# Kernel optimization log

Hardware: AMD Instinct MI355X
Metric: run time of the kernel (lower is better)

Reference implementation:

```python
import jax, jax.numpy as jnp
import numpy as np
import math

B, SQ, SK, D_MODEL, OUT_DIM = 8, 2048, 2048, 1024, 128
MASK_VALUE = -1e6  # torch code fills masked scores with -1000000.0, not -inf


def setup_inputs() -> dict:
    key = jax.random.key(0)
    ks = jax.random.split(key, 10)
    scale = 1.0 / math.sqrt(D_MODEL)
    return {
        "queries": jax.random.normal(ks[0], (B, SQ, D_MODEL), dtype=jnp.float32),
        "keys": jax.random.normal(ks[1], (B, SK, D_MODEL), dtype=jnp.float32),
        "values": jax.random.normal(ks[2], (B, SK, D_MODEL), dtype=jnp.float32),
        "valid_lens": jax.random.randint(ks[3], (B,), 1, SK + 1, dtype=jnp.int32),
        "w_q": jax.random.normal(ks[4], (D_MODEL, OUT_DIM), dtype=jnp.float32) * scale,
        "b_q": jnp.zeros((OUT_DIM,), dtype=jnp.float32),
        "w_k": jax.random.normal(ks[5], (D_MODEL, OUT_DIM), dtype=jnp.float32) * scale,
        "b_k": jnp.zeros((OUT_DIM,), dtype=jnp.float32),
        "w_v": jax.random.normal(ks[6], (D_MODEL, OUT_DIM), dtype=jnp.float32) * scale,
        "b_v": jnp.zeros((OUT_DIM,), dtype=jnp.float32),
    }


def reference(queries, keys, values, valid_lens, w_q, b_q, w_k, b_k, w_v, b_v):
    # QKV projections (LazyLinear equivalents)
    Q = queries @ w_q + b_q   # [B, SQ, OUT_DIM]
    K = keys @ w_k + b_k      # [B, SK, OUT_DIM]
    V = values @ w_v + b_v    # [B, SK, OUT_DIM]
    dim = Q.shape[-1]
    scores = jnp.einsum("bqd,bkd->bqk", Q, K) / jnp.sqrt(jnp.asarray(dim, Q.dtype))
    # masked_softmax: valid_lens [B] -> mask positions >= valid_len on the key axis
    mask = jnp.arange(scores.shape[-1])[None, None, :] < valid_lens[:, None, None]
    scores = jnp.where(mask, scores, jnp.asarray(MASK_VALUE, scores.dtype))
    attn = jax.nn.softmax(scores, axis=-1)
    return jnp.einsum("bqk,bkd->bqd", attn, V)  # [B, SQ, OUT_DIM]
```

## Files before the change

### kernel.cpp

```cpp
#include <hip/hip_runtime.h>
#include <math.h>

constexpr int BATCH  = 8;
constexpr int SEQQ   = 2048;
constexpr int SEQK   = 2048;
constexpr int DMODEL = 1024;
constexpr int ODIM   = 128;
constexpr int KSPLIT = 2;

typedef __attribute__((ext_vector_type(8))) short bf16x8;
typedef __attribute__((ext_vector_type(4))) float f32x4;

__device__ inline unsigned short f2bf(float f) {
    union { float f; unsigned int u; } v; v.f = f;
    unsigned int r = v.u + 0x7FFFu + ((v.u >> 16) & 1u);
    return (unsigned short)(r >> 16);
}

__device__ __forceinline__ void gl_lds16(const void* g, void* l) {
    __builtin_amdgcn_global_load_lds(
        (const __attribute__((address_space(1))) unsigned int*)g,
        (__attribute__((address_space(3))) unsigned int*)l, 16, 0, 0);
}

__global__ __launch_bounds__(256)
void wtrans_kernel(const float* __restrict__ Wq, const float* __restrict__ Wk,
                   const float* __restrict__ Wv, unsigned short* __restrict__ Wt)
{
    const int which = blockIdx.z;
    const float* __restrict__ W = which == 0 ? Wq : (which == 1 ? Wk : Wv);
    unsigned short* __restrict__ dst = Wt + (size_t)which * DMODEL * ODIM;
    const int k0 = blockIdx.x * 32, n0 = blockIdx.y * 32;
    __shared__ unsigned short T[32][36];
    const int t = threadIdx.x;
    const int r = t >> 3, c = (t & 7) * 4;
    float4 w = *(const float4*)(W + (size_t)(k0 + r) * ODIM + n0 + c);
    T[r][c + 0] = f2bf(w.x); T[r][c + 1] = f2bf(w.y);
    T[r][c + 2] = f2bf(w.z); T[r][c + 3] = f2bf(w.w);
    __syncthreads();
    const int n = t >> 3, k4 = (t & 7) * 4;
    ushort4 o;
    o.x = T[k4 + 0][n]; o.y = T[k4 + 1][n];
    o.z = T[k4 + 2][n]; o.w = T[k4 + 3][n];
    *(ushort4*)(dst + (size_t)(n0 + n) * DMODEL + k0 + k4) = o;
}

__global__ __launch_bounds__(256)
void proj_kernel(const float* __restrict__ Aq, const float* __restrict__ Ak,
                 const float* __restrict__ Av,
                 const unsigned short* __restrict__ Wt_all,
                 const float* __restrict__ bq, const float* __restrict__ bk,
                 const float* __restrict__ bv,
                 unsigned short* __restrict__ Qb, unsigned short* __restrict__ Kb,
                 unsigned short* __restrict__ Vt)
{
    const int which = blockIdx.y;
    const float* __restrict__ A    = which == 0 ? Aq : (which == 1 ? Ak : Av);
    const float* __restrict__ bias = which == 0 ? bq : (which == 1 ? bk : bv);
    const unsigned short* __restrict__ Wt = Wt_all + (size_t)which * DMODEL * ODIM;

    const int row0 = blockIdx.x * 64;
    const int t = threadIdx.x, wave = t >> 6, lane = t & 63;
    const int lrow = lane & 15, quad = lane >> 4;

    __shared__ __align__(16) float          As[64][64];
    __shared__ __align__(16) unsigned short Ws[128][64];

    f32x4 acc[8];
#pragma unroll
    for (int nt = 0; nt < 8; ++nt)
#pragma unroll
        for (int i = 0; i < 4; ++i) acc[nt][i] = 0.f;

    const float* agp[4]; float* aldst[4];
    const unsigned short* wgp[4]; unsigned short* wldst[4];
#pragma unroll
    for (int j = 0; j < 4; ++j) {
        const int s = wave * 256 + j * 64 + lane;
        const int ar = s >> 4, ac = s & 15, ag = ac ^ (ar & 7);
        agp[j]   = A + (size_t)(row0 + ar) * DMODEL + ag * 4;
        aldst[j] = &((float*)As)[s * 4];
        const int wr = s >> 3, wc = s & 7, wg = wc ^ (wr & 7);
        wgp[j]   = Wt + (size_t)wr * DMODEL + wg * 8;
        wldst[j] = &((unsigned short*)Ws)[s * 8];
    }

    const int R = wave * 16 + lrow;
    const int x3 = lrow & 7;

    for (int k0 = 0; k0 < DMODEL; k0 += 64) {
#pragma unroll
        for (int j = 0; j < 4; ++j) {
            gl_lds16(agp[j] + k0, aldst[j]);
            gl_lds16(wgp[j] + k0, wldst[j]);
        }
        __syncthreads();
#pragma unroll
        for (int ks = 0; ks < 2; ++ks) {
            const int c0 = ks * 8 + quad * 2;
            float4 a0 = *(const float4*)&As[R][(c0 ^ x3) * 4];
            float4 a1 = *(const float4*)&As[R][((c0 + 1) ^ x3) * 4];
            bf16x8 af;
            af[0] = (short)f2bf(a0.x); af[1] = (short)f2bf(a0.y);
            af[2] = (short)f2bf(a0.z); af[3] = (short)f2bf(a0.w);
            af[4] = (short)f2bf(a1.x); af[5] = (short)f2bf(a1.y);
            af[6] = (short)f2bf(a1.z); af[7] = (short)f2bf(a1.w);
#pragma unroll
            for (int nt = 0; nt < 8; ++nt) {
                const int n = nt * 16 + lrow;
                const int c = (ks * 4 + quad) ^ x3;
                bf16x8 bfr = *(const bf16x8*)&Ws[n][c * 8];
                acc[nt] = __builtin_amdgcn_mfma_f32_16x16x32_bf16(af, bfr, acc[nt], 0, 0, 0);
            }
        }
        __syncthreads();
    }

    const float sc = (which == 0) ? 0.08838834764831845f : 1.0f;
    float bv_[8];
#pragma unroll
    for (int nt = 0; nt < 8; ++nt) bv_[nt] = bias[nt * 16 + lrow];

    const int b  = row0 >> 11;
    const int mb = row0 & 2047;

    if (which == 2) {
#pragma unroll
        for (int nt = 0; nt < 8; ++nt) {
            const int n = nt * 16 + lrow;
            ushort4 o;
            o.x = f2bf(acc[nt][0] + bv_[nt]);
            o.y = f2bf(acc[nt][1] + bv_[nt]);
            o.z = f2bf(acc[nt][2] + bv_[nt]);
            o.w = f2bf(acc[nt][3] + bv_[nt]);
            *(ushort4*)(Vt + ((size_t)b * ODIM + n) * SEQK + mb + wave * 16 + quad * 4) = o;
        }
    } else {
        unsigned short* __restrict__ Ob = (which == 0) ? Qb : Kb;
#pragma unroll
        for (int nt = 0; nt < 8; ++nt)
#pragma unroll
            for (int r = 0; r < 4; ++r) {
                float val = sc * (acc[nt][r] + bv_[nt]);
                Ob[(size_t)(row0 + wave * 16 + quad * 4 + r) * ODIM + nt * 16 + lrow] = f2bf(val);
            }
    }
}

__global__ __launch_bounds__(256)
void flash_kernel(const unsigned short* __restrict__ Qb,
                  const unsigned short* __restrict__ Kb,
                  const unsigned short* __restrict__ Vt,
                  const int* __restrict__ valid_lens,
                  float* __restrict__ Op, float* __restrict__ Lp)
{
    const int b = blockIdx.y, s = blockIdx.z, q0 = blockIdx.x * 64;
    const int t = threadIdx.x, wave = t >> 6, lane = t & 63;
    const int lrow = lane & 15, quad = lane >> 4;
    const int SKH = SEQK / KSPLIT;

    const int valid = valid_lens[b];
    const int vloc  = min(valid - s * SKH, SKH);

    float* __restrict__ opart = Op + ((size_t)(s * BATCH + b) * SEQQ + q0) * ODIM;
    float* __restrict__ lpart = Lp + (size_t)(s * BATCH + b) * SEQQ + q0;

    if (vloc <= 0) {
        float4 z = {0.f, 0.f, 0.f, 0.f};
#pragma unroll
        for (int i = 0; i < 8; ++i) ((float4*)opart)[i * 256 + t] = z;
        if (t < 64) lpart[t] = 0.f;
        return;
    }

    __shared__ __align__(16) unsigned short Ks[64][136];
    __shared__ __align__(16) unsigned short Vs[128][72];
    __shared__ __align__(16) unsigned short Ps[4][16][72];

    bf16x8 qf[4];
    {
        const unsigned short* qptr =
            Qb + ((size_t)b * SEQQ + q0 + wave * 16 + lrow) * ODIM + quad * 8;
#pragma unroll
        for (int ks = 0; ks < 4; ++ks) qf[ks] = *(const bf16x8*)(qptr + ks * 32);
    }

    f32x4 o[8];
#pragma unroll
    for (int nt = 0; nt < 8; ++nt)
#pragma unroll
        for (int i = 0; i < 4; ++i) o[nt][i] = 0.f;
    float lsum[4] = {0.f, 0.f, 0.f, 0.f};

    const unsigned short* kbase = Kb + ((size_t)b * SEQK + s * SKH) * ODIM;
    const unsigned short* vbase = Vt + (size_t)b * ODIM * SEQK + s * SKH;

    const int kr = t >> 2, kc = (t & 3) * 32;
    const int vr = t >> 1, vc = (t & 1) * 32;
    const int nch = (vloc + 63) >> 6;

    for (int c = 0; c < nch; ++c) {
        const int k0 = c * 64;
        {
            const unsigned short* ksrc = kbase + (size_t)(k0 + kr) * ODIM + kc;
            const unsigned short* vsrc = vbase + (size_t)vr * SEQK + k0 + vc;
#pragma unroll
            for (int i = 0; i < 4; ++i) {
                *(int4*)&Ks[kr][kc + i * 8] = *(const int4*)(ksrc + i * 8);
                *(int4*)&Vs[vr][vc + i * 8] = *(const int4*)(vsrc + i * 8);
            }
        }
        __syncthreads();

        f32x4 sv[4];
#pragma unroll
        for (int nt = 0; nt < 4; ++nt)
#pragma unroll
            for (int i = 0; i < 4; ++i) sv[nt][i] = 0.f;
#pragma unroll
        for (int ks = 0; ks < 4; ++ks)
#pragma unroll
            for (int nt = 0; nt < 4; ++nt) {
                bf16x8 kf = *(const bf16x8*)&Ks[nt * 16 + lrow][ks * 32 + quad * 8];
                sv[nt] = __builtin_amdgcn_mfma_f32_16x16x32_bf16(qf[ks], kf, sv[nt], 0, 0, 0);
            }

        if (k0 + 64 > vloc) {
#pragma unroll
            for (int nt = 0; nt < 4; ++nt)
                if (k0 + nt * 16 + lrow >= vloc) {
#pragma unroll
                    for (int i = 0; i < 4; ++i) sv[nt][i] = -1e30f;
                }
        }

#pragma unroll
        for (int nt = 0; nt < 4; ++nt)
#pragma unroll
            for (int r = 0; r < 4; ++r) {
                float p = __expf(sv[nt][r]);
                lsum[r] += p;
                Ps[wave][quad * 4 + r][nt * 16 + lrow] = f2bf(p);
            }

        bf16x8 pf0 = *(const bf16x8*)&Ps[wave][lrow][quad * 8];
        bf16x8 pf1 = *(const bf16x8*)&Ps[wave][lrow][32 + quad * 8];

#pragma unroll
        for (int nt = 0; nt < 8; ++nt) {
            bf16x8 vf0 = *(const bf16x8*)&Vs[nt * 16 + lrow][quad * 8];
            o[nt] = __builtin_amdgcn_mfma_f32_16x16x32_bf16(pf0, vf0, o[nt], 0, 0, 0);
        }
#pragma unroll
        for (int nt = 0; nt < 8; ++nt) {
            bf16x8 vf1 = *(const bf16x8*)&Vs[nt * 16 + lrow][32 + quad * 8];
            o[nt] = __builtin_amdgcn_mfma_f32_16x16x32_bf16(pf1, vf1, o[nt], 0, 0, 0);
        }
        __syncthreads();
    }

#pragma unroll
    for (int msk = 1; msk < 16; msk <<= 1)
#pragma unroll
        for (int r = 0; r < 4; ++r) lsum[r] += __shfl_xor(lsum[r], msk);
    if (lrow == 0) {
#pragma unroll
        for (int r = 0; r < 4; ++r)
            lpart[wave * 16 + quad * 4 + r] = lsum[r];
    }

#pragma unroll
    for (int nt = 0; nt < 8; ++nt)
#pragma unroll
        for (int r = 0; r < 4; ++r)
            opart[(size_t)(wave * 16 + quad * 4 + r) * ODIM + nt * 16 + lrow] = o[nt][r];
}

__global__ __launch_bounds__(256)
void combine_kernel(const float* __restrict__ Op, const float* __restrict__ Lp,
                    float* __restrict__ out)
{
    const int idx = blockIdx.x * 256 + threadIdx.x;
    const int row = idx >> 5;
    const size_t stride = (size_t)BATCH * SEQQ;
    float l = Lp[row] + Lp[stride + row];
    const float inv = 1.f / l;
    float4 a = ((const float4*)Op)[idx];
    float4 c = ((const float4*)(Op + stride * ODIM))[idx];
    float4 r;
    r.x = (a.x + c.x) * inv; r.y = (a.y + c.y) * inv;
    r.z = (a.z + c.z) * inv; r.w = (a.w + c.w) * inv;
    ((float4*)out)[idx] = r;
}

extern "C" void kernel_launch(void* const* d_in, const int* in_sizes, int n_in,
                              void* d_out, int out_size, void* d_ws, size_t ws_size,
                              hipStream_t stream)
{
    const float* queries    = (const float*)d_in[0];
    const float* keys       = (const float*)d_in[1];
    const float* values     = (const float*)d_in[2];
    const int*   valid_lens = (const int*)d_in[3];
    const float* w_q        = (const float*)d_in[4];
    const float* b_q        = (const float*)d_in[5];
    const float* w_k        = (const float*)d_in[6];
    const float* b_k        = (const float*)d_in[7];
    const float* w_v        = (const float*)d_in[8];
    const float* b_v        = (const float*)d_in[9];
    float* out = (float*)d_out;

    const size_t nQKV = (size_t)BATCH * SEQQ * ODIM;
    unsigned short* Qb = (unsigned short*)d_ws;
    unsigned short* Kb = Qb + nQKV;
    unsigned short* Vt = Kb + nQKV;
    unsigned short* Wt = Vt + nQKV;
    float* Op = (float*)(Wt + (size_t)3 * DMODEL * ODIM);
    float* Lp = Op + (size_t)KSPLIT * nQKV;

    wtrans_kernel<<<dim3(DMODEL / 32, ODIM / 32, 3), 256, 0, stream>>>(w_q, w_k, w_v, Wt);

    proj_kernel<<<dim3((BATCH * SEQQ) / 64, 3), 256, 0, stream>>>(
        queries, keys, values, Wt, b_q, b_k, b_v, Qb, Kb, Vt);

    flash_kernel<<<dim3(SEQQ / 64, BATCH, KSPLIT), 256, 0, stream>>>(
        Qb, Kb, Vt, valid_lens, Op, Lp);

    combine_kernel<<<(BATCH * SEQQ * ODIM / 4) / 256, 256, 0, stream>>>(Op, Lp, out);
}
```

Measured before the change: 266.9 us.

## Drop LDS staging in projection and flash kernels, widen tiles, split keys four ways

The projection kernel stops staging A and W through LDS and reads fragments straight from global memory. Each wave now computes a 32x64 tile and uses a packed round-to-bf16 conversion. The flash kernel handles 128 query rows per block (32 per wave), reads K and V fragments directly from global memory with no block barriers, and splits the key axis four ways when workspace allows. Fully masked splits skip writing the O partials, and the combine kernel ignores splits whose row sum is zero. The aim is to cut LDS traffic and barriers and to increase parallelism, at the cost of more L2/global traffic from uncoalesced fragment loads and a larger combine pass.

```diff
diff --git a/kernel.cpp b/kernel.cpp
--- a/kernel.cpp
+++ b/kernel.cpp
@@ -6,7 +6,6 @@
 constexpr int SEQK   = 2048;
 constexpr int DMODEL = 1024;
 constexpr int ODIM   = 128;
-constexpr int KSPLIT = 2;
 
 typedef __attribute__((ext_vector_type(8))) short bf16x8;
 typedef __attribute__((ext_vector_type(4))) float f32x4;
@@ -17,10 +16,10 @@
     return (unsigned short)(r >> 16);
 }
 
-__device__ __forceinline__ void gl_lds16(const void* g, void* l) {
-    __builtin_amdgcn_global_load_lds(
-        (const __attribute__((address_space(1))) unsigned int*)g,
-        (__attribute__((address_space(3))) unsigned int*)l, 16, 0, 0);
+__device__ __forceinline__ unsigned int pk2bf(float a, float b) {
+    unsigned int ua = __float_as_uint(a) + 0x8000u;
+    unsigned int ub = __float_as_uint(b) + 0x8000u;
+    return __builtin_amdgcn_perm(ub, ua, 0x07060302u);
 }
 
 __global__ __launch_bounds__(256)
@@ -62,167 +61,152 @@
     const int row0 = blockIdx.x * 64;
     const int t = threadIdx.x, wave = t >> 6, lane = t & 63;
     const int lrow = lane & 15, quad = lane >> 4;
-
-    __shared__ __align__(16) float          As[64][64];
-    __shared__ __align__(16) unsigned short Ws[128][64];
-
-    f32x4 acc[8];
-#pragma unroll
-    for (int nt = 0; nt < 8; ++nt)
-#pragma unroll
-        for (int i = 0; i < 4; ++i) acc[nt][i] = 0.f;
-
-    const float* agp[4]; float* aldst[4];
-    const unsigned short* wgp[4]; unsigned short* wldst[4];
-#pragma unroll
-    for (int j = 0; j < 4; ++j) {
-        const int s = wave * 256 + j * 64 + lane;
-        const int ar = s >> 4, ac = s & 15, ag = ac ^ (ar & 7);
-        agp[j]   = A + (size_t)(row0 + ar) * DMODEL + ag * 4;
-        aldst[j] = &((float*)As)[s * 4];
-        const int wr = s >> 3, wc = s & 7, wg = wc ^ (wr & 7);
-        wgp[j]   = Wt + (size_t)wr * DMODEL + wg * 8;
-        wldst[j] = &((unsigned short*)Ws)[s * 8];
-    }
-
-    const int R = wave * 16 + lrow;
-    const int x3 = lrow & 7;
-
-    for (int k0 = 0; k0 < DMODEL; k0 += 64) {
-#pragma unroll
-        for (int j = 0; j < 4; ++j) {
-            gl_lds16(agp[j] + k0, aldst[j]);
-            gl_lds16(wgp[j] + k0, wldst[j]);
+    const int mh = (wave & 1) * 32;
+    const int nh = (wave >> 1) * 64;
+
+    const float* a0 = A + (size_t)(row0 + mh + lrow) * DMODEL + quad * 8;
+    const float* a1 = a0 + (size_t)16 * DMODEL;
+    const unsigned short* w0 = Wt + (size_t)(nh + lrow) * DMODEL + quad * 8;
+
+    f32x4 acc[2][4];
+#pragma unroll
+    for (int mt = 0; mt < 2; ++mt)
+#pragma unroll
+        for (int nt = 0; nt < 4; ++nt)
+#pragma unroll
+            for (int i = 0; i < 4; ++i) acc[mt][nt][i] = 0.f;
+
+#pragma unroll 4
+    for (int k0 = 0; k0 < DMODEL; k0 += 32) {
+        float4 x0 = *(const float4*)(a0 + k0);
+        float4 x1 = *(const float4*)(a0 + k0 + 4);
+        float4 y0 = *(const float4*)(a1 + k0);
+        float4 y1 = *(const float4*)(a1 + k0 + 4);
+        bf16x8 af0, af1;
+        ((unsigned int*)&af0)[0] = pk2bf(x0.x, x0.y);
+        ((unsigned int*)&af0)[1] = pk2bf(x0.z, x0.w);
+        ((unsigned int*)&af0)[2] = pk2bf(x1.x, x1.y);
+        ((unsigned int*)&af0)[3] = pk2bf(x1.z, x1.w);
+        ((unsigned int*)&af1)[0] = pk2bf(y0.x, y0.y);
+        ((unsigned int*)&af1)[1] = pk2bf(y0.z, y0.w);
+        ((unsigned int*)&af1)[2] = pk2bf(y1.x, y1.y);
+        ((unsigned int*)&af1)[3] = pk2bf(y1.z, y1.w);
+#pragma unroll
+        for (int nt = 0; nt < 4; ++nt) {
+            bf16x8 wf = *(const bf16x8*)(w0 + (size_t)nt * 16 * DMODEL + k0);
+            acc[0][nt] = __builtin_amdgcn_mfma_f32_16x16x32_bf16(af0, wf, acc[0][nt], 0, 0, 0);
+            acc[1][nt] = __builtin_amdgcn_mfma_f32_16x16x32_bf16(af1, wf, acc[1][nt], 0, 0, 0);
         }
-        __syncthreads();
-#pragma unroll
-        for (int ks = 0; ks < 2; ++ks) {
-            const int c0 = ks * 8 + quad * 2;
-            float4 a0 = *(const float4*)&As[R][(c0 ^ x3) * 4];
-            float4 a1 = *(const float4*)&As[R][((c0 + 1) ^ x3) * 4];
-            bf16x8 af;
-            af[0] = (short)f2bf(a0.x); af[1] = (short)f2bf(a0.y);
-            af[2] = (short)f2bf(a0.z); af[3] = (short)f2bf(a0.w);
-            af[4] = (short)f2bf(a1.x); af[5] = (short)f2bf(a1.y);
-            af[6] = (short)f2bf(a1.z); af[7] = (short)f2bf(a1.w);
-#pragma unroll
-            for (int nt = 0; nt < 8; ++nt) {
-                const int n = nt * 16 + lrow;
-                const int c = (ks * 4 + quad) ^ x3;
-                bf16x8 bfr = *(const bf16x8*)&Ws[n][c * 8];
-                acc[nt] = __builtin_amdgcn_mfma_f32_16x16x32_bf16(af, bfr, acc[nt], 0, 0, 0);
-            }
-        }
-        __syncthreads();
     }
 
     const float sc = (which == 0) ? 0.08838834764831845f : 1.0f;
-    float bv_[8];
-#pragma unroll
-    for (int nt = 0; nt < 8; ++nt) bv_[nt] = bias[nt * 16 + lrow];
+    float bv_[4];
+#pragma unroll
+    for (int nt = 0; nt < 4; ++nt) bv_[nt] = bias[nh + nt * 16 + lrow];
 
     const int b  = row0 >> 11;
     const int mb = row0 & 2047;
 
     if (which == 2) {
 #pragma unroll
-        for (int nt = 0; nt < 8; ++nt) {
-            const int n = nt * 16 + lrow;
-            ushort4 o;
-            o.x = f2bf(acc[nt][0] + bv_[nt]);
-            o.y = f2bf(acc[nt][1] + bv_[nt]);
-            o.z = f2bf(acc[nt][2] + bv_[nt]);
-            o.w = f2bf(acc[nt][3] + bv_[nt]);
-            *(ushort4*)(Vt + ((size_t)b * ODIM + n) * SEQK + mb + wave * 16 + quad * 4) = o;
-        }
+        for (int mt = 0; mt < 2; ++mt)
+#pragma unroll
+            for (int nt = 0; nt < 4; ++nt) {
+                const int n = nh + nt * 16 + lrow;
+                ushort4 o;
+                o.x = f2bf(acc[mt][nt][0] + bv_[nt]);
+                o.y = f2bf(acc[mt][nt][1] + bv_[nt]);
+                o.z = f2bf(acc[mt][nt][2] + bv_[nt]);
+                o.w = f2bf(acc[mt][nt][3] + bv_[nt]);
+                *(ushort4*)(Vt + ((size_t)b * ODIM + n) * SEQK
+                            + mb + mh + mt * 16 + quad * 4) = o;
+            }
     } else {
         unsigned short* __restrict__ Ob = (which == 0) ? Qb : Kb;
 #pragma unroll
-        for (int nt = 0; nt < 8; ++nt)
-#pragma unroll
-            for (int r = 0; r < 4; ++r) {
-                float val = sc * (acc[nt][r] + bv_[nt]);
-                Ob[(size_t)(row0 + wave * 16 + quad * 4 + r) * ODIM + nt * 16 + lrow] = f2bf(val);
-            }
-    }
-}
-
-__global__ __launch_bounds__(256)
+        for (int mt = 0; mt < 2; ++mt)
+#pragma unroll
+            for (int nt = 0; nt < 4; ++nt)
+#pragma unroll
+                for (int r = 0; r < 4; ++r) {
+                    float val = sc * (acc[mt][nt][r] + bv_[nt]);
+                    Ob[(size_t)(row0 + mh + mt * 16 + quad * 4 + r) * ODIM
+                       + nh + nt * 16 + lrow] = f2bf(val);
+                }
+    }
+}
+
+__global__ __launch_bounds__(256, 2)
 void flash_kernel(const unsigned short* __restrict__ Qb,
                   const unsigned short* __restrict__ Kb,
                   const unsigned short* __restrict__ Vt,
                   const int* __restrict__ valid_lens,
-                  float* __restrict__ Op, float* __restrict__ Lp)
-{
-    const int b = blockIdx.y, s = blockIdx.z, q0 = blockIdx.x * 64;
+                  float* __restrict__ Op, float* __restrict__ Lp, int nsplit)
+{
+    const int b = blockIdx.y, s = blockIdx.z, q0 = blockIdx.x * 128;
+    const int skh = SEQK / nsplit;
     const int t = threadIdx.x, wave = t >> 6, lane = t & 63;
     const int lrow = lane & 15, quad = lane >> 4;
-    const int SKH = SEQK / KSPLIT;
 
     const int valid = valid_lens[b];
-    const int vloc  = min(valid - s * SKH, SKH);
-
+    const int vloc  = min(valid - s * skh, skh);
+
+    float* __restrict__ lpart = Lp + (size_t)(s * BATCH + b) * SEQQ + q0;
     float* __restrict__ opart = Op + ((size_t)(s * BATCH + b) * SEQQ + q0) * ODIM;
-    float* __restrict__ lpart = Lp + (size_t)(s * BATCH + b) * SEQQ + q0;
 
     if (vloc <= 0) {
-        float4 z = {0.f, 0.f, 0.f, 0.f};
-#pragma unroll
-        for (int i = 0; i < 8; ++i) ((float4*)opart)[i * 256 + t] = z;
-        if (t < 64) lpart[t] = 0.f;
+        if (lane < 32) lpart[wave * 32 + lane] = 0.f;
         return;
     }
 
-    __shared__ __align__(16) unsigned short Ks[64][136];
-    __shared__ __align__(16) unsigned short Vs[128][72];
-    __shared__ __align__(16) unsigned short Ps[4][16][72];
-
-    bf16x8 qf[4];
+    __shared__ __align__(16) unsigned short Ps[4][32][72];
+
+    const int r0 = q0 + wave * 32;
+
+    bf16x8 qf[2][4];
     {
-        const unsigned short* qptr =
-            Qb + ((size_t)b * SEQQ + q0 + wave * 16 + lrow) * ODIM + quad * 8;
-#pragma unroll
-        for (int ks = 0; ks < 4; ++ks) qf[ks] = *(const bf16x8*)(qptr + ks * 32);
-    }
-
-    f32x4 o[8];
-#pragma unroll
-    for (int nt = 0; nt < 8; ++nt)
-#pragma unroll
-        for (int i = 0; i < 4; ++i) o[nt][i] = 0.f;
-    float lsum[4] = {0.f, 0.f, 0.f, 0.f};
-
-    const unsigned short* kbase = Kb + ((size_t)b * SEQK + s * SKH) * ODIM;
-    const unsigned short* vbase = Vt + (size_t)b * ODIM * SEQK + s * SKH;
-
-    const int kr = t >> 2, kc = (t & 3) * 32;
-    const int vr = t >> 1, vc = (t & 1) * 32;
+        const unsigned short* qp =
+            Qb + ((size_t)b * SEQQ + r0 + lrow) * ODIM + quad * 8;
+#pragma unroll
+        for (int mt = 0; mt < 2; ++mt)
+#pragma unroll
+            for (int ks = 0; ks < 4; ++ks)
+                qf[mt][ks] = *(const bf16x8*)(qp + (size_t)mt * 16 * ODIM + ks * 32);
+    }
+
+    f32x4 o[2][8];
+#pragma unroll
+    for (int mt = 0; mt < 2; ++mt)
+#pragma unroll
+        for (int nt = 0; nt < 8; ++nt)
+#pragma unroll
+            for (int i = 0; i < 4; ++i) o[mt][nt][i] = 0.f;
+    float lsum[2][4] = {{0.f, 0.f, 0.f, 0.f}, {0.f, 0.f, 0.f, 0.f}};
+
+    const unsigned short* kb =
+        Kb + ((size_t)b * SEQK + s * skh + lrow) * ODIM + quad * 8;
+    const unsigned short* vb =
+        Vt + (size_t)b * ODIM * SEQK + (size_t)lrow * SEQK + s * skh + quad * 8;
+
     const int nch = (vloc + 63) >> 6;
 
     for (int c = 0; c < nch; ++c) {
         const int k0 = c * 64;
-        {
-            const unsigned short* ksrc = kbase + (size_t)(k0 + kr) * ODIM + kc;
-            const unsigned short* vsrc = vbase + (size_t)vr * SEQK + k0 + vc;
-#pragma unroll
-            for (int i = 0; i < 4; ++i) {
-                *(int4*)&Ks[kr][kc + i * 8] = *(const int4*)(ksrc + i * 8);
-                *(int4*)&Vs[vr][vc + i * 8] = *(const int4*)(vsrc + i * 8);
-            }
-        }
-        __syncthreads();
-
-        f32x4 sv[4];
-#pragma unroll
-        for (int nt = 0; nt < 4; ++nt)
-#pragma unroll
-            for (int i = 0; i < 4; ++i) sv[nt][i] = 0.f;
+
+        f32x4 sv[2][4];
+#pragma unroll
+        for (int mt = 0; mt < 2; ++mt)
+#pragma unroll
+            for (int nt = 0; nt < 4; ++nt)
+#pragma unroll
+                for (int i = 0; i < 4; ++i) sv[mt][nt][i] = 0.f;
 #pragma unroll
         for (int ks = 0; ks < 4; ++ks)
 #pragma unroll
             for (int nt = 0; nt < 4; ++nt) {
-                bf16x8 kf = *(const bf16x8*)&Ks[nt * 16 + lrow][ks * 32 + quad * 8];
-                sv[nt] = __builtin_amdgcn_mfma_f32_16x16x32_bf16(qf[ks], kf, sv[nt], 0, 0, 0);
+                bf16x8 kf = *(const bf16x8*)(kb + (size_t)(k0 + nt * 16) * ODIM + ks * 32);
+                sv[0][nt] = __builtin_amdgcn_mfma_f32_16x16x32_bf16(qf[0][ks], kf, sv[0][nt], 0, 0, 0);
+                sv[1][nt] = __builtin_amdgcn_mfma_f32_16x16x32_bf16(qf[1][ks], kf, sv[1][nt], 0, 0, 0);
             }
 
         if (k0 + 64 > vloc) {
@@ -230,66 +214,83 @@
             for (int nt = 0; nt < 4; ++nt)
                 if (k0 + nt * 16 + lrow >= vloc) {
 #pragma unroll
-                    for (int i = 0; i < 4; ++i) sv[nt][i] = -1e30f;
+                    for (int i = 0; i < 4; ++i) { sv[0][nt][i] = -1e30f; sv[1][nt][i] = -1e30f; }
                 }
         }
 
 #pragma unroll
-        for (int nt = 0; nt < 4; ++nt)
-#pragma unroll
-            for (int r = 0; r < 4; ++r) {
-                float p = __expf(sv[nt][r]);
-                lsum[r] += p;
-                Ps[wave][quad * 4 + r][nt * 16 + lrow] = f2bf(p);
+        for (int mt = 0; mt < 2; ++mt)
+#pragma unroll
+            for (int nt = 0; nt < 4; ++nt)
+#pragma unroll
+                for (int r = 0; r < 4; ++r) {
+                    float p = __expf(sv[mt][nt][r]);
+                    lsum[mt][r] += p;
+                    Ps[wave][mt * 16 + quad * 4 + r][nt * 16 + lrow] =
+                        (unsigned short)((__float_as_uint(p) + 0x8000u) >> 16);
+                }
+
+        bf16x8 pf[2][2];
+#pragma unroll
+        for (int mt = 0; mt < 2; ++mt) {
+            pf[mt][0] = *(const bf16x8*)&Ps[wave][mt * 16 + lrow][quad * 8];
+            pf[mt][1] = *(const bf16x8*)&Ps[wave][mt * 16 + lrow][32 + quad * 8];
+        }
+
+#pragma unroll
+        for (int k2 = 0; k2 < 2; ++k2)
+#pragma unroll
+            for (int nt = 0; nt < 8; ++nt) {
+                bf16x8 vf = *(const bf16x8*)(vb + (size_t)(nt * 16) * SEQK + k0 + k2 * 32);
+                o[0][nt] = __builtin_amdgcn_mfma_f32_16x16x32_bf16(pf[0][k2], vf, o[0][nt], 0, 0, 0);
+                o[1][nt] = __builtin_amdgcn_mfma_f32_16x16x32_bf16(pf[1][k2], vf, o[1][nt], 0, 0, 0);
             }
-
-        bf16x8 pf0 = *(const bf16x8*)&Ps[wave][lrow][quad * 8];
-        bf16x8 pf1 = *(const bf16x8*)&Ps[wave][lrow][32 + quad * 8];
-
-#pragma unroll
-        for (int nt = 0; nt < 8; ++nt) {
-            bf16x8 vf0 = *(const bf16x8*)&Vs[nt * 16 + lrow][quad * 8];
-            o[nt] = __builtin_amdgcn_mfma_f32_16x16x32_bf16(pf0, vf0, o[nt], 0, 0, 0);
-        }
-#pragma unroll
-        for (int nt = 0; nt < 8; ++nt) {
-            bf16x8 vf1 = *(const bf16x8*)&Vs[nt * 16 + lrow][32 + quad * 8];
-            o[nt] = __builtin_amdgcn_mfma_f32_16x16x32_bf16(pf1, vf1, o[nt], 0, 0, 0);
-        }
-        __syncthreads();
     }
 
 #pragma unroll
     for (int msk = 1; msk < 16; msk <<= 1)
 #pragma unroll
-        for (int r = 0; r < 4; ++r) lsum[r] += __shfl_xor(lsum[r], msk);
+        for (int mt = 0; mt < 2; ++mt)
+#pragma unroll
+            for (int r = 0; r < 4; ++r) lsum[mt][r] += __shfl_xor(lsum[mt][r], msk);
     if (lrow == 0) {
 #pragma unroll
-        for (int r = 0; r < 4; ++r)
-            lpart[wave * 16 + quad * 4 + r] = lsum[r];
-    }
-
-#pragma unroll
-    for (int nt = 0; nt < 8; ++nt)
-#pragma unroll
-        for (int r = 0; r < 4; ++r)
-            opart[(size_t)(wave * 16 + quad * 4 + r) * ODIM + nt * 16 + lrow] = o[nt][r];
+        for (int mt = 0; mt < 2; ++mt)
+#pragma unroll
+            for (int r = 0; r < 4; ++r)
+                lpart[wave * 32 + mt * 16 + quad * 4 + r] = lsum[mt][r];
+    }
+
+#pragma unroll
+    for (int mt = 0; mt < 2; ++mt)
+#pragma unroll
+        for (int nt = 0; nt < 8; ++nt)
+#pragma unroll
+            for (int r = 0; r < 4; ++r)
+                opart[(size_t)(wave * 32 + mt * 16 + quad * 4 + r) * ODIM
+                      + nt * 16 + lrow] = o[mt][nt][r];
 }
 
 __global__ __launch_bounds__(256)
 void combine_kernel(const float* __restrict__ Op, const float* __restrict__ Lp,
-                    float* __restrict__ out)
+                    float* __restrict__ out, int nsplit)
 {
     const int idx = blockIdx.x * 256 + threadIdx.x;
     const int row = idx >> 5;
-    const size_t stride = (size_t)BATCH * SEQQ;
-    float l = Lp[row] + Lp[stride + row];
+    const size_t SL = (size_t)BATCH * SEQQ;
+    float l = 0.f;
+    float4 acc = {0.f, 0.f, 0.f, 0.f};
+    for (int s = 0; s < nsplit; ++s) {
+        float ls = Lp[(size_t)s * SL + row];
+        if (ls > 0.f) {
+            float4 v = ((const float4*)(Op + (size_t)s * SL * ODIM))[idx];
+            acc.x += v.x; acc.y += v.y; acc.z += v.z; acc.w += v.w;
+            l += ls;
+        }
+    }
     const float inv = 1.f / l;
-    float4 a = ((const float4*)Op)[idx];
-    float4 c = ((const float4*)(Op + stride * ODIM))[idx];
     float4 r;
-    r.x = (a.x + c.x) * inv; r.y = (a.y + c.y) * inv;
-    r.z = (a.z + c.z) * inv; r.w = (a.w + c.w) * inv;
+    r.x = acc.x * inv; r.y = acc.y * inv; r.z = acc.z * inv; r.w = acc.w * inv;
     ((float4*)out)[idx] = r;
 }
 
@@ -314,16 +315,22 @@
     unsigned short* Kb = Qb + nQKV;
     unsigned short* Vt = Kb + nQKV;
     unsigned short* Wt = Vt + nQKV;
-    float* Op = (float*)(Wt + (size_t)3 * DMODEL * ODIM);
-    float* Lp = Op + (size_t)KSPLIT * nQKV;
+    const size_t base = 3 * nQKV * sizeof(unsigned short)
+                      + (size_t)3 * DMODEL * ODIM * sizeof(unsigned short);
+
+    int KS = 4;
+    if (ws_size < base + 4 * (nQKV * 4 + (size_t)BATCH * SEQQ * 4)) KS = 2;
+
+    float* Op = (float*)((char*)d_ws + base);
+    float* Lp = Op + (size_t)KS * nQKV;
 
     wtrans_kernel<<<dim3(DMODEL / 32, ODIM / 32, 3), 256, 0, stream>>>(w_q, w_k, w_v, Wt);
 
     proj_kernel<<<dim3((BATCH * SEQQ) / 64, 3), 256, 0, stream>>>(
         queries, keys, values, Wt, b_q, b_k, b_v, Qb, Kb, Vt);
 
-    flash_kernel<<<dim3(SEQQ / 64, BATCH, KSPLIT), 256, 0, stream>>>(
-        Qb, Kb, Vt, valid_lens, Op, Lp);
-
-    combine_kernel<<<(BATCH * SEQQ * ODIM / 4) / 256, 256, 0, stream>>>(Op, Lp, out);
-}
+    flash_kernel<<<dim3(SEQQ / 128, BATCH, KS), 256, 0, stream>>>(
+        Qb, Kb, Vt, valid_lens, Op, Lp, KS);
+
+    combine_kernel<<<(BATCH * SEQQ * ODIM / 4) / 256, 256, 0, stream>>>(Op, Lp, out, KS);
+}
```

New measurement: 330.6 us. 23.9% more time.

## Shrink projection tiles, split keys four ways, async-load K/V with swizzled LDS

Applied to the files above, without the earlier changes.

The projection kernel now uses 32-row tiles, with waves split across M and N, and packs bf16 with perm instructions. The flash kernel loads K and V via global_load_lds into XOR-swizzled unpadded LDS, and splits the key range four ways when workspace allows. Empty splits skip writing zeros, and combine skips them by checking the partial sum. Occupancy hints are added to both kernels. This trades more partial-output traffic in combine for more parallelism and less load latency. The bf16 rounding also changes from round-to-nearest-even to round-half-up.

```diff
diff --git a/kernel.cpp b/kernel.cpp
--- a/kernel.cpp
+++ b/kernel.cpp
@@ -6,7 +6,6 @@
 constexpr int SEQK   = 2048;
 constexpr int DMODEL = 1024;
 constexpr int ODIM   = 128;
-constexpr int KSPLIT = 2;
 
 typedef __attribute__((ext_vector_type(8))) short bf16x8;
 typedef __attribute__((ext_vector_type(4))) float f32x4;
@@ -15,6 +14,12 @@
     union { float f; unsigned int u; } v; v.f = f;
     unsigned int r = v.u + 0x7FFFu + ((v.u >> 16) & 1u);
     return (unsigned short)(r >> 16);
+}
+
+__device__ __forceinline__ unsigned int pk2bf(float a, float b) {
+    unsigned int ua = __float_as_uint(a) + 0x8000u;
+    unsigned int ub = __float_as_uint(b) + 0x8000u;
+    return __builtin_amdgcn_perm(ub, ua, 0x07060302u);
 }
 
 __device__ __forceinline__ void gl_lds16(const void* g, void* l) {
@@ -45,7 +50,7 @@
     *(ushort4*)(dst + (size_t)(n0 + n) * DMODEL + k0 + k4) = o;
 }
 
-__global__ __launch_bounds__(256)
+__global__ __launch_bounds__(256, 6)
 void proj_kernel(const float* __restrict__ Aq, const float* __restrict__ Ak,
                  const float* __restrict__ Av,
                  const unsigned short* __restrict__ Wt_all,
@@ -59,130 +64,134 @@
     const float* __restrict__ bias = which == 0 ? bq : (which == 1 ? bk : bv);
     const unsigned short* __restrict__ Wt = Wt_all + (size_t)which * DMODEL * ODIM;
 
-    const int row0 = blockIdx.x * 64;
+    const int row0 = blockIdx.x * 32;
     const int t = threadIdx.x, wave = t >> 6, lane = t & 63;
     const int lrow = lane & 15, quad = lane >> 4;
-
-    __shared__ __align__(16) float          As[64][64];
-    __shared__ __align__(16) unsigned short Ws[128][64];
-
-    f32x4 acc[8];
-#pragma unroll
-    for (int nt = 0; nt < 8; ++nt)
+    const int mh = (wave & 1) * 16;
+    const int nh = (wave >> 1) * 64;
+
+    __shared__ __align__(16) float          As[32 * 64];
+    __shared__ __align__(16) unsigned short Ws[128 * 64];
+
+    f32x4 acc[4];
+#pragma unroll
+    for (int nt = 0; nt < 4; ++nt)
 #pragma unroll
         for (int i = 0; i < 4; ++i) acc[nt][i] = 0.f;
 
-    const float* agp[4]; float* aldst[4];
+    const float* agp[2]; float* aldst[2];
     const unsigned short* wgp[4]; unsigned short* wldst[4];
 #pragma unroll
+    for (int j = 0; j < 2; ++j) {
+        const int s = j * 256 + t;
+        const int ar = s >> 4, ac = (s & 15) ^ (ar & 15);
+        agp[j]   = A + (size_t)(row0 + ar) * DMODEL + ac * 4;
+        aldst[j] = &As[s * 4];
+    }
+#pragma unroll
     for (int j = 0; j < 4; ++j) {
-        const int s = wave * 256 + j * 64 + lane;
-        const int ar = s >> 4, ac = s & 15, ag = ac ^ (ar & 7);
-        agp[j]   = A + (size_t)(row0 + ar) * DMODEL + ag * 4;
-        aldst[j] = &((float*)As)[s * 4];
-        const int wr = s >> 3, wc = s & 7, wg = wc ^ (wr & 7);
-        wgp[j]   = Wt + (size_t)wr * DMODEL + wg * 8;
-        wldst[j] = &((unsigned short*)Ws)[s * 8];
-    }
-
-    const int R = wave * 16 + lrow;
+        const int s = j * 256 + t;
+        const int wr = s >> 3, wc = (s & 7) ^ (wr & 7);
+        wgp[j]   = Wt + (size_t)wr * DMODEL + wc * 8;
+        wldst[j] = &Ws[s * 8];
+    }
+
+    const int R = mh + lrow;
+    const int x4 = lrow;
     const int x3 = lrow & 7;
 
     for (int k0 = 0; k0 < DMODEL; k0 += 64) {
 #pragma unroll
-        for (int j = 0; j < 4; ++j) {
-            gl_lds16(agp[j] + k0, aldst[j]);
-            gl_lds16(wgp[j] + k0, wldst[j]);
-        }
+        for (int j = 0; j < 2; ++j) gl_lds16(agp[j] + k0, aldst[j]);
+#pragma unroll
+        for (int j = 0; j < 4; ++j) gl_lds16(wgp[j] + k0, wldst[j]);
         __syncthreads();
 #pragma unroll
         for (int ks = 0; ks < 2; ++ks) {
             const int c0 = ks * 8 + quad * 2;
-            float4 a0 = *(const float4*)&As[R][(c0 ^ x3) * 4];
-            float4 a1 = *(const float4*)&As[R][((c0 + 1) ^ x3) * 4];
+            float4 a0 = *(const float4*)&As[(R * 16 + (c0 ^ x4)) * 4];
+            float4 a1 = *(const float4*)&As[(R * 16 + ((c0 + 1) ^ x4)) * 4];
             bf16x8 af;
-            af[0] = (short)f2bf(a0.x); af[1] = (short)f2bf(a0.y);
-            af[2] = (short)f2bf(a0.z); af[3] = (short)f2bf(a0.w);
-            af[4] = (short)f2bf(a1.x); af[5] = (short)f2bf(a1.y);
-            af[6] = (short)f2bf(a1.z); af[7] = (short)f2bf(a1.w);
-#pragma unroll
-            for (int nt = 0; nt < 8; ++nt) {
-                const int n = nt * 16 + lrow;
+            ((unsigned int*)&af)[0] = pk2bf(a0.x, a0.y);
+            ((unsigned int*)&af)[1] = pk2bf(a0.z, a0.w);
+            ((unsigned int*)&af)[2] = pk2bf(a1.x, a1.y);
+            ((unsigned int*)&af)[3] = pk2bf(a1.z, a1.w);
+#pragma unroll
+            for (int nt = 0; nt < 4; ++nt) {
+                const int n = nh + nt * 16 + lrow;
                 const int c = (ks * 4 + quad) ^ x3;
-                bf16x8 bfr = *(const bf16x8*)&Ws[n][c * 8];
-                acc[nt] = __builtin_amdgcn_mfma_f32_16x16x32_bf16(af, bfr, acc[nt], 0, 0, 0);
+                bf16x8 wf = *(const bf16x8*)&Ws[(n * 8 + c) * 8];
+                acc[nt] = __builtin_amdgcn_mfma_f32_16x16x32_bf16(af, wf, acc[nt], 0, 0, 0);
             }
         }
         __syncthreads();
     }
 
     const float sc = (which == 0) ? 0.08838834764831845f : 1.0f;
-    float bv_[8];
-#pragma unroll
-    for (int nt = 0; nt < 8; ++nt) bv_[nt] = bias[nt * 16 + lrow];
+    float bv_[4];
+#pragma unroll
+    for (int nt = 0; nt < 4; ++nt) bv_[nt] = bias[nh + nt * 16 + lrow];
 
     const int b  = row0 >> 11;
     const int mb = row0 & 2047;
 
     if (which == 2) {
 #pragma unroll
-        for (int nt = 0; nt < 8; ++nt) {
-            const int n = nt * 16 + lrow;
+        for (int nt = 0; nt < 4; ++nt) {
+            const int n = nh + nt * 16 + lrow;
             ushort4 o;
             o.x = f2bf(acc[nt][0] + bv_[nt]);
             o.y = f2bf(acc[nt][1] + bv_[nt]);
             o.z = f2bf(acc[nt][2] + bv_[nt]);
             o.w = f2bf(acc[nt][3] + bv_[nt]);
-            *(ushort4*)(Vt + ((size_t)b * ODIM + n) * SEQK + mb + wave * 16 + quad * 4) = o;
+            *(ushort4*)(Vt + ((size_t)b * ODIM + n) * SEQK + mb + mh + quad * 4) = o;
         }
     } else {
         unsigned short* __restrict__ Ob = (which == 0) ? Qb : Kb;
 #pragma unroll
-        for (int nt = 0; nt < 8; ++nt)
+        for (int nt = 0; nt < 4; ++nt)
 #pragma unroll
             for (int r = 0; r < 4; ++r) {
                 float val = sc * (acc[nt][r] + bv_[nt]);
-                Ob[(size_t)(row0 + wave * 16 + quad * 4 + r) * ODIM + nt * 16 + lrow] = f2bf(val);
+                Ob[(size_t)(row0 + mh + quad * 4 + r) * ODIM + nh + nt * 16 + lrow]
+                    = f2bf(val);
             }
     }
 }
 
-__global__ __launch_bounds__(256)
+__global__ __launch_bounds__(256, 3)
 void flash_kernel(const unsigned short* __restrict__ Qb,
                   const unsigned short* __restrict__ Kb,
                   const unsigned short* __restrict__ Vt,
                   const int* __restrict__ valid_lens,
-                  float* __restrict__ Op, float* __restrict__ Lp)
+                  float* __restrict__ Op, float* __restrict__ Lp, int nsplit)
 {
     const int b = blockIdx.y, s = blockIdx.z, q0 = blockIdx.x * 64;
+    const int skh = SEQK / nsplit;
     const int t = threadIdx.x, wave = t >> 6, lane = t & 63;
     const int lrow = lane & 15, quad = lane >> 4;
-    const int SKH = SEQK / KSPLIT;
 
     const int valid = valid_lens[b];
-    const int vloc  = min(valid - s * SKH, SKH);
-
+    const int vloc  = min(valid - s * skh, skh);
+
+    float* __restrict__ lpart = Lp + (size_t)(s * BATCH + b) * SEQQ + q0;
     float* __restrict__ opart = Op + ((size_t)(s * BATCH + b) * SEQQ + q0) * ODIM;
-    float* __restrict__ lpart = Lp + (size_t)(s * BATCH + b) * SEQQ + q0;
 
     if (vloc <= 0) {
-        float4 z = {0.f, 0.f, 0.f, 0.f};
-#pragma unroll
-        for (int i = 0; i < 8; ++i) ((float4*)opart)[i * 256 + t] = z;
         if (t < 64) lpart[t] = 0.f;
         return;
     }
 
-    __shared__ __align__(16) unsigned short Ks[64][136];
-    __shared__ __align__(16) unsigned short Vs[128][72];
+    __shared__ __align__(16) unsigned short Ks[64 * 128];
+    __shared__ __align__(16) unsigned short Vs[128 * 64];
     __shared__ __align__(16) unsigned short Ps[4][16][72];
 
     bf16x8 qf[4];
     {
-        const unsigned short* qptr =
+        const unsigned short* qp =
             Qb + ((size_t)b * SEQQ + q0 + wave * 16 + lrow) * ODIM + quad * 8;
 #pragma unroll
-        for (int ks = 0; ks < 4; ++ks) qf[ks] = *(const bf16x8*)(qptr + ks * 32);
+        for (int ks = 0; ks < 4; ++ks) qf[ks] = *(const bf16x8*)(qp + ks * 32);
     }
 
     f32x4 o[8];
@@ -192,23 +201,30 @@
         for (int i = 0; i < 4; ++i) o[nt][i] = 0.f;
     float lsum[4] = {0.f, 0.f, 0.f, 0.f};
 
-    const unsigned short* kbase = Kb + ((size_t)b * SEQK + s * SKH) * ODIM;
-    const unsigned short* vbase = Vt + (size_t)b * ODIM * SEQK + s * SKH;
-
-    const int kr = t >> 2, kc = (t & 3) * 32;
-    const int vr = t >> 1, vc = (t & 1) * 32;
+    const unsigned short* kgp[4]; unsigned short* kldst[4];
+    const unsigned short* vgp[4]; unsigned short* vldst[4];
+    const unsigned short* kbase = Kb + ((size_t)b * SEQK + s * skh) * ODIM;
+    const unsigned short* vbase = Vt + (size_t)b * ODIM * SEQK + s * skh;
+#pragma unroll
+    for (int j = 0; j < 4; ++j) {
+        const int sl = j * 256 + t;
+        const int kr = sl >> 4, kc = (sl & 15) ^ (kr & 15);
+        kgp[j]   = kbase + (size_t)kr * ODIM + kc * 8;
+        kldst[j] = &Ks[sl * 8];
+        const int vr = sl >> 3, vc = (sl & 7) ^ (vr & 7);
+        vgp[j]   = vbase + (size_t)vr * SEQK + vc * 8;
+        vldst[j] = &Vs[sl * 8];
+    }
+
+    const int x4 = lrow, x3 = lrow & 7;
     const int nch = (vloc + 63) >> 6;
 
     for (int c = 0; c < nch; ++c) {
         const int k0 = c * 64;
-        {
-            const unsigned short* ksrc = kbase + (size_t)(k0 + kr) * ODIM + kc;
-            const unsigned short* vsrc = vbase + (size_t)vr * SEQK + k0 + vc;
-#pragma unroll
-            for (int i = 0; i < 4; ++i) {
-                *(int4*)&Ks[kr][kc + i * 8] = *(const int4*)(ksrc + i * 8);
-                *(int4*)&Vs[vr][vc + i * 8] = *(const int4*)(vsrc + i * 8);
-            }
+#pragma unroll
+        for (int j = 0; j < 4; ++j) {
+            gl_lds16(kgp[j] + (size_t)k0 * ODIM, kldst[j]);
+            gl_lds16(vgp[j] + k0, vldst[j]);
         }
         __syncthreads();
 
@@ -221,7 +237,9 @@
         for (int ks = 0; ks < 4; ++ks)
 #pragma unroll
             for (int nt = 0; nt < 4; ++nt) {
-                bf16x8 kf = *(const bf16x8*)&Ks[nt * 16 + lrow][ks * 32 + quad * 8];
+                const int kr = nt * 16 + lrow;
+                const int cc = (ks * 4 + quad) ^ x4;
+                bf16x8 kf = *(const bf16x8*)&Ks[(kr * 16 + cc) * 8];
                 sv[nt] = __builtin_amdgcn_mfma_f32_16x16x32_bf16(qf[ks], kf, sv[nt], 0, 0, 0);
             }
 
@@ -240,7 +258,8 @@
             for (int r = 0; r < 4; ++r) {
                 float p = __expf(sv[nt][r]);
                 lsum[r] += p;
-                Ps[wave][quad * 4 + r][nt * 16 + lrow] = f2bf(p);
+                Ps[wave][quad * 4 + r][nt * 16 + lrow] =
+                    (unsigned short)((__float_as_uint(p) + 0x8000u) >> 16);
             }
 
         bf16x8 pf0 = *(const bf16x8*)&Ps[wave][lrow][quad * 8];
@@ -248,13 +267,15 @@
 
 #pragma unroll
         for (int nt = 0; nt < 8; ++nt) {
-            bf16x8 vf0 = *(const bf16x8*)&Vs[nt * 16 + lrow][quad * 8];
-            o[nt] = __builtin_amdgcn_mfma_f32_16x16x32_bf16(pf0, vf0, o[nt], 0, 0, 0);
+            const int vrow = nt * 16 + lrow;
+            bf16x8 v0 = *(const bf16x8*)&Vs[(vrow * 8 + (quad ^ x3)) * 8];
+            o[nt] = __builtin_amdgcn_mfma_f32_16x16x32_bf16(pf0, v0, o[nt], 0, 0, 0);
         }
 #pragma unroll
         for (int nt = 0; nt < 8; ++nt) {
-            bf16x8 vf1 = *(const bf16x8*)&Vs[nt * 16 + lrow][32 + quad * 8];
-            o[nt] = __builtin_amdgcn_mfma_f32_16x16x32_bf16(pf1, vf1, o[nt], 0, 0, 0);
+            const int vrow = nt * 16 + lrow;
+            bf16x8 v1 = *(const bf16x8*)&Vs[(vrow * 8 + ((4 + quad) ^ x3)) * 8];
+            o[nt] = __builtin_amdgcn_mfma_f32_16x16x32_bf16(pf1, v1, o[nt], 0, 0, 0);
         }
         __syncthreads();
     }
@@ -273,23 +294,30 @@
     for (int nt = 0; nt < 8; ++nt)
 #pragma unroll
         for (int r = 0; r < 4; ++r)
-            opart[(size_t)(wave * 16 + quad * 4 + r) * ODIM + nt * 16 + lrow] = o[nt][r];
+            opart[(size_t)(wave * 16 + quad * 4 + r) * ODIM + nt * 16 + lrow]
+                = o[nt][r];
 }
 
 __global__ __launch_bounds__(256)
 void combine_kernel(const float* __restrict__ Op, const float* __restrict__ Lp,
-                    float* __restrict__ out)
+                    float* __restrict__ out, int nsplit)
 {
     const int idx = blockIdx.x * 256 + threadIdx.x;
     const int row = idx >> 5;
-    const size_t stride = (size_t)BATCH * SEQQ;
-    float l = Lp[row] + Lp[stride + row];
+    const size_t SL = (size_t)BATCH * SEQQ;
+    float l = 0.f;
+    float4 acc = {0.f, 0.f, 0.f, 0.f};
+    for (int s = 0; s < nsplit; ++s) {
+        float ls = Lp[(size_t)s * SL + row];
+        if (ls > 0.f) {
+            float4 v = ((const float4*)(Op + (size_t)s * SL * ODIM))[idx];
+            acc.x += v.x; acc.y += v.y; acc.z += v.z; acc.w += v.w;
+            l += ls;
+        }
+    }
     const float inv = 1.f / l;
-    float4 a = ((const float4*)Op)[idx];
-    float4 c = ((const float4*)(Op + stride * ODIM))[idx];
     float4 r;
-    r.x = (a.x + c.x) * inv; r.y = (a.y + c.y) * inv;
-    r.z = (a.z + c.z) * inv; r.w = (a.w + c.w) * inv;
+    r.x = acc.x * inv; r.y = acc.y * inv; r.z = acc.z * inv; r.w = acc.w * inv;
     ((float4*)out)[idx] = r;
 }
 
@@ -314,16 +342,22 @@
     unsigned short* Kb = Qb + nQKV;
     unsigned short* Vt = Kb + nQKV;
     unsigned short* Wt = Vt + nQKV;
-    float* Op = (float*)(Wt + (size_t)3 * DMODEL * ODIM);
-    float* Lp = Op + (size_t)KSPLIT * nQKV;
+    const size_t base = 3 * nQKV * sizeof(unsigned short)
+                      + (size_t)3 * DMODEL * ODIM * sizeof(unsigned short);
+
+    int KS = 4;
+    if (ws_size < base + 4 * (nQKV * 4 + (size_t)BATCH * SEQQ * 4)) KS = 2;
+
+    float* Op = (float*)((char*)d_ws + base);
+    float* Lp = Op + (size_t)KS * nQKV;
 
     wtrans_kernel<<<dim3(DMODEL / 32, ODIM / 32, 3), 256, 0, stream>>>(w_q, w_k, w_v, Wt);
 
-    proj_kernel<<<dim3((BATCH * SEQQ) / 64, 3), 256, 0, stream>>>(
+    proj_kernel<<<dim3((BATCH * SEQQ) / 32, 3), 256, 0, stream>>>(
         queries, keys, values, Wt, b_q, b_k, b_v, Qb, Kb, Vt);
 
-    flash_kernel<<<dim3(SEQQ / 64, BATCH, KSPLIT), 256, 0, stream>>>(
-        Qb, Kb, Vt, valid_lens, Op, Lp);
-
-    combine_kernel<<<(BATCH * SEQQ * ODIM / 4) / 256, 256, 0, stream>>>(Op, Lp, out);
-}
+    flash_kernel<<<dim3(SEQQ / 64, BATCH, KS), 256, 0, stream>>>(
+        Qb, Kb, Vt, valid_lens, Op, Lp, KS);
+
+    combine_kernel<<<(BATCH * SEQQ * ODIM / 4) / 256, 256, 0, stream>>>(Op, Lp, out, KS);
+}
```

Result: faster. 256.9 us (-3.8%).
